# Kernel optimization log

Hardware: AMD Instinct MI355X
Metric: run time of the kernel (lower is better)

The kernel has to match this reference:

```python
import jax, jax.numpy as jnp
import numpy as np

OUTPUT_SIZES = [1, 3, 6, 8]  # SPP pyramid -> total KV length 110

def _bounds(n, out):
    # PyTorch AdaptiveMaxPool2d bin boundaries
    return [((i * n) // out, -((-(i + 1) * n) // out)) for i in range(out)]

def adaptive_max_pool2d(x, out):
    # x: [B, C, H, W] -> [B, C, out, out]
    B, C, H, W = x.shape
    rows = jnp.stack([x[:, :, s:e, :].max(axis=2) for s, e in _bounds(H, out)], axis=2)
    return jnp.stack([rows[:, :, :, s:e].max(axis=3) for s, e in _bounds(W, out)], axis=3)

def spp(x):
    # [B, C, H, W] -> [B, C, S] with S = sum(o*o) = 110
    B, C = x.shape[:2]
    return jnp.concatenate(
        [adaptive_max_pool2d(x, o).reshape(B, C, o * o) for o in OUTPUT_SIZES], axis=2)

def conv1x1(x, w):
    # 1x1 conv, no bias: w [O, C], x [B, C, H, W]
    return jnp.einsum('oc,bchw->bohw', w, x)

def setup_inputs() -> dict:
    key = jax.random.key(0)
    ks = jax.random.split(key, 6)
    B, C, H, W = 16, 512, 64, 64
    IC = C // 2
    x = jax.random.normal(ks[0], (B, C, H, W), jnp.float32)
    y = jax.random.normal(ks[1], (B, C, H, W), jnp.float32)
    sc = 1.0 / np.sqrt(C)
    w_phi = jax.random.normal(ks[2], (IC, C), jnp.float32) * sc
    w_theta = jax.random.normal(ks[3], (IC, C), jnp.float32) * sc
    w_g = jax.random.normal(ks[4], (IC, C), jnp.float32) * sc
    w_mask = jax.random.normal(ks[5], (C, IC), jnp.float32) * (1.0 / np.sqrt(IC))
    return {"x": x, "y": y, "w_phi": w_phi, "w_theta": w_theta,
            "w_g": w_g, "w_mask": w_mask}

def reference(x, y, w_phi, w_theta, w_g, w_mask):
    B, C, H, W = x.shape
    IC = w_phi.shape[0]
    N = H * W
    # Query: [B, N, IC]
    x_phi = conv1x1(x, w_phi).reshape(B, IC, N).transpose(0, 2, 1)
    # Keys/values from SPP-pooled y: [B, IC, S] / [B, S, IC]
    y_theta = spp(conv1x1(y, w_theta))
    y_g = spp(conv1x1(y, w_g)).transpose(0, 2, 1)
    # Attention with softmax over the QUERY axis (dim=1), as in the source
    attn = jax.nn.softmax(jnp.einsum('bnc,bcs->bns', x_phi, y_theta), axis=1)
    agg = jnp.einsum('bns,bsc->bnc', attn, y_g)          # [B, N, IC]
    agg = agg.transpose(0, 2, 1).reshape(B, IC, H, W)     # [B, IC, H, W]
    mask = conv1x1(agg, w_mask)                           # [B, C, H, W]
    return mask + x
```

## Files before the change

### kernel.cpp

```cpp
#include <hip/hip_runtime.h>

#define DI __device__ __forceinline__

typedef __attribute__((ext_vector_type(8))) __bf16 bf16x8;
typedef __attribute__((ext_vector_type(4))) float f32x4;

DI unsigned short f2bf(float x) {
  union { float f; unsigned u; } v; v.f = x;
  unsigned r = v.u + 0x7fffu + ((v.u >> 16) & 1u);
  return (unsigned short)(r >> 16);
}
DI float bf2f(unsigned short h) {
  union { unsigned u; float f; } v; v.u = ((unsigned)h) << 16;
  return v.f;
}
DI unsigned pack2(float a, float b) {
  return (unsigned)f2bf(a) | (((unsigned)f2bf(b)) << 16);
}

DI void gl_lds16(const void* g, void* l) {
  __builtin_amdgcn_global_load_lds(
      (const __attribute__((address_space(1))) void*)g,
      (__attribute__((address_space(3))) void*)l, 16, 0, 0);
}

DI void wt_vm0()  { asm volatile("s_waitcnt vmcnt(0) lgkmcnt(0)" ::: "memory"); }
DI void wt_vm6()  { asm volatile("s_waitcnt vmcnt(6) lgkmcnt(0)" ::: "memory"); }
DI void wt_vm8()  { asm volatile("s_waitcnt vmcnt(8) lgkmcnt(0)" ::: "memory"); }
DI void wt_vm10() { asm volatile("s_waitcnt vmcnt(10) lgkmcnt(0)" ::: "memory"); }
DI void wt_vm12() { asm volatile("s_waitcnt vmcnt(12) lgkmcnt(0)" ::: "memory"); }

__global__ __launch_bounds__(256) void pw_conv(
    const float* __restrict__ w_theta, const float* __restrict__ w_g,
    unsigned short* __restrict__ wTG)
{
  int e = (blockIdx.x * 256 + threadIdx.x) * 8;
  const float* src = (e < 131072) ? (w_theta + e) : (w_g + (e - 131072));
  float4 a = *(const float4*)src;
  float4 c = *(const float4*)(src + 4);
  uint4 u;
  u.x = pack2(a.x, a.y); u.y = pack2(a.z, a.w);
  u.z = pack2(c.x, c.y); u.w = pack2(c.z, c.w);
  *(uint4*)(wTG + e) = u;
}

__constant__ int c_RS[18] = {0, 0,21,42, 0,10,21,32,42,53, 0,8,16,24,32,40,48,56};
__constant__ int c_RE[18] = {64, 22,43,64, 11,22,32,43,54,64, 8,16,24,32,40,48,56,64};

__global__ __launch_bounds__(256) void k1f_conv_pool(
    const float* __restrict__ y, const unsigned short* __restrict__ wTG,
    unsigned short* __restrict__ Rbuf)
{
  const int tid = threadIdx.x;
  const int id = blockIdx.x;
  const int tile = (id & 7) * 16 + (id >> 3);
  const int mb = (tile & 3) * 128;
  const int nbt = tile >> 2;
  const int nb = nbt * 128;
  const int b  = blockIdx.y;
  const int lane = tid & 63, wv = tid >> 6;
  const int wm = (wv & 1) * 64, wn = (wv >> 1) * 64;
  const int l15 = lane & 15, l4 = lane >> 4;

  __shared__ __align__(16) char smem[3 * 18432];
  float* P = (float*)smem;

  const int c4 = tid & 7, n4 = tid >> 3;
  const float* ycol = y + ((size_t)(b * 512)) * 4096 + nb + n4 * 4;

  f32x4 acc[4][4];
  #pragma unroll
  for (int i = 0; i < 4; ++i)
    #pragma unroll
    for (int j = 0; j < 4; ++j) acc[i][j] = f32x4{0.f, 0.f, 0.f, 0.f};

  float xr0[16], xr1[16];
  auto yload = [&](float* xr, int kb) {
    #pragma unroll
    for (int cc = 0; cc < 4; ++cc)
      *(float4*)&xr[cc * 4] =
          *(const float4*)(ycol + (size_t)(kb + c4 * 4 + cc) * 4096);
  };
  auto dmaA = [&](int buf, int kb) {
    unsigned short* As = (unsigned short*)(smem + buf * 18432);
    #pragma unroll
    for (int p = 0; p < 2; ++p) {
      int chunk = (wv * 2 + p) * 64 + lane;
      int row = chunk >> 2, cc16 = chunk & 3;
      gl_lds16(wTG + ((size_t)(mb + row)) * 512 + kb + cc16 * 8,
               As + (wv * 2 + p) * 512);
    }
  };
  auto bwrite = [&](int buf, const float* xr) {
    unsigned short* Bs = (unsigned short*)(smem + buf * 18432 + 8192);
    #pragma unroll
    for (int q = 0; q < 4; ++q) {
      uint2 u;
      u.x = pack2(xr[q], xr[4 + q]);
      u.y = pack2(xr[8 + q], xr[12 + q]);
      *(uint2*)&Bs[(n4 * 4 + q) * 40 + c4 * 4] = u;
    }
  };
  auto mfma_step = [&](int buf) {
    const unsigned short* As = (const unsigned short*)(smem + buf * 18432);
    const unsigned short* Bs = As + 4096;
    bf16x8 af[4], bfr[4];
    #pragma unroll
    for (int i = 0; i < 4; ++i)
      af[i] = *(const bf16x8*)&As[(wm + i * 16 + l15) * 32 + l4 * 8];
    #pragma unroll
    for (int j = 0; j < 4; ++j)
      bfr[j] = *(const bf16x8*)&Bs[(wn + j * 16 + l15) * 40 + l4 * 8];
    #pragma unroll
    for (int i = 0; i < 4; ++i)
      #pragma unroll
      for (int j = 0; j < 4; ++j)
        acc[i][j] = __builtin_amdgcn_mfma_f32_16x16x32_bf16(af[i], bfr[j], acc[i][j], 0, 0, 0);
  };

  yload(xr0, 0);
  dmaA(0, 0);
  bwrite(0, xr0);
  yload(xr1, 32);
  #pragma unroll
  for (int t = 0; t < 16; ++t) {
    if (t + 1 < 16) dmaA((t + 1) % 3, (t + 1) * 32);
    if (t + 2 < 16) yload((t & 1) ? xr1 : xr0, (t + 2) * 32);
    if (t < 14) wt_vm10();
    else if (t == 14) wt_vm6();
    else wt_vm0();
    __builtin_amdgcn_s_barrier();
    __builtin_amdgcn_sched_barrier(0);
    mfma_step(t % 3);
    if (t + 1 < 16) bwrite((t + 1) % 3, (t & 1) ? xr0 : xr1);
  }

  const int hloc = wv >> 1;
  #pragma unroll
  for (int pass = 0; pass < 2; ++pass) {
    __syncthreads();
    if (hloc == pass) {
      #pragma unroll
      for (int i = 0; i < 4; ++i)
        #pragma unroll
        for (int j = 0; j < 4; ++j)
          #pragma unroll
          for (int r = 0; r < 4; ++r)
            P[(wm + i * 16 + l4 * 4 + r) * 65 + j * 16 + l15] = acc[i][j][r];
    }
    __syncthreads();
    const int o = tid & 127;
    size_t rbase = (((size_t)(b * 64 + nbt * 2 + pass)) * 18) * 512 + mb + o;
    if (tid < 128) {
      float b0 = -3.4e38f, b1 = b0, b2 = b0, b3 = b0;
      #pragma unroll
      for (int w = 0; w < 64; ++w) {
        float v = P[o * 65 + w];
        b0 = fmaxf(b0, v);
        if (w < 22) b1 = fmaxf(b1, v);
        if (w >= 21 && w < 43) b2 = fmaxf(b2, v);
        if (w >= 42) b3 = fmaxf(b3, v);
      }
      Rbuf[rbase]           = f2bf(b0);
      Rbuf[rbase + 512]     = f2bf(b1);
      Rbuf[rbase + 2 * 512] = f2bf(b2);
      Rbuf[rbase + 3 * 512] = f2bf(b3);
    } else {
      float s6[6], s8[8];
      #pragma unroll
      for (int i = 0; i < 6; ++i) s6[i] = -3.4e38f;
      #pragma unroll
      for (int i = 0; i < 8; ++i) s8[i] = -3.4e38f;
      constexpr int R6S[6] = {0, 10, 21, 32, 42, 53};
      constexpr int R6E[6] = {11, 22, 32, 43, 54, 64};
      #pragma unroll
      for (int w = 0; w < 64; ++w) {
        float v = P[o * 65 + w];
        #pragma unroll
        for (int i = 0; i < 6; ++i)
          if (w >= R6S[i] && w < R6E[i]) s6[i] = fmaxf(s6[i], v);
        s8[w >> 3] = fmaxf(s8[w >> 3], v);
      }
      #pragma unroll
      for (int i = 0; i < 6; ++i) Rbuf[rbase + (size_t)(4 + i) * 512] = f2bf(s6[i]);
      #pragma unroll
      for (int i = 0; i < 8; ++i) Rbuf[rbase + (size_t)(10 + i) * 512] = f2bf(s8[i]);
    }
  }
}

__global__ __launch_bounds__(256) void k2_pool_final(
    const unsigned short* __restrict__ Rbuf, float* __restrict__ Pt,
    float* __restrict__ Pg)
{
  const int s = blockIdx.x, b = blockIdx.y, tid = threadIdx.x;
  size_t obase = ((size_t)(b * 128) + s) * 256 + tid;
  if (s >= 110) { Pt[obase] = 0.f; Pg[obase] = 0.f; return; }
  int he, wb;
  if (s == 0)      { he = 0; wb = 0; }
  else if (s < 10) { int i = s - 1;  he = 1 + i / 3;  wb = 1 + i % 3; }
  else if (s < 46) { int i = s - 10; he = 4 + i / 6;  wb = 4 + i % 6; }
  else             { int i = s - 46; he = 10 + i / 8; wb = 10 + i % 8; }
  float m0 = -3.4e38f, m1 = -3.4e38f;
  int e = c_RE[he];
  for (int h = c_RS[he]; h < e; ++h) {
    const unsigned short* r = Rbuf + (((size_t)(b * 64 + h)) * 18 + wb) * 512;
    m0 = fmaxf(m0, bf2f(r[tid]));
    m1 = fmaxf(m1, bf2f(r[tid + 256]));
  }
  Pt[obase] = m0;
  Pg[obase] = m1;
}

__global__ __launch_bounds__(256) void k3_fused(
    const float* __restrict__ Pt, const float* __restrict__ Pg,
    const float* __restrict__ w_phi, const float* __restrict__ w_mask,
    unsigned short* __restrict__ Kth, unsigned short* __restrict__ Ktl,
    unsigned short* __restrict__ Vb)
{
  __shared__ __align__(16) char sm3[51200];
  const int tid = threadIdx.x;
  const int tx = tid & 15, ty = tid >> 4;
  const int b = blockIdx.y;
  if (blockIdx.z == 0) {
    const int ct = blockIdx.x;
    const int c0 = tx * 4, s0 = ty * 8;
    float* Ls = (float*)sm3;
    float* Ws = Ls + 128 * 64;
    float acc[8][4] = {};
    for (int kc = 0; kc < 256; kc += 64) {
      #pragma unroll
      for (int j = 0; j < 8; ++j) {
        int flat = tid + 256 * j;
        int row = flat >> 4, k4 = (flat & 15) << 2;
        *(float4*)&Ls[row * 64 + k4] =
            *(const float4*)(Pt + ((size_t)(b * 128) + row) * 256 + kc + k4);
      }
      #pragma unroll
      for (int j = 0; j < 4; ++j) {
        int flat = tid + 256 * j;
        int row = flat >> 4, cc4 = (flat & 15) << 2;
        *(float4*)&Ws[row * 68 + cc4] =
            *(const float4*)(w_phi + (size_t)(kc + row) * 512 + ct * 64 + cc4);
      }
      __syncthreads();
      for (int k = 0; k < 64; k += 4) {
        float4 wv[4];
        #pragma unroll
        for (int kk = 0; kk < 4; ++kk) wv[kk] = *(const float4*)&Ws[(k + kk) * 68 + c0];
        #pragma unroll
        for (int i = 0; i < 8; ++i) {
          float4 a = *(const float4*)&Ls[(s0 + i) * 64 + k];
          const float* ap = (const float*)&a;
          #pragma unroll
          for (int kk = 0; kk < 4; ++kk) {
            const float* wp = (const float*)&wv[kk];
            acc[i][0] += ap[kk] * wp[0];
            acc[i][1] += ap[kk] * wp[1];
            acc[i][2] += ap[kk] * wp[2];
            acc[i][3] += ap[kk] * wp[3];
          }
        }
      }
      __syncthreads();
    }
    #pragma unroll
    for (int i = 0; i < 8; ++i) {
      unsigned short hi[4]; float lo[4];
      #pragma unroll
      for (int j = 0; j < 4; ++j) { hi[j] = f2bf(acc[i][j]); lo[j] = acc[i][j] - bf2f(hi[j]); }
      size_t base = ((size_t)(b * 128) + s0 + i) * 512 + ct * 64 + c0;
      uint2 uh; uh.x = (unsigned)hi[0] | ((unsigned)hi[1] << 16);
      uh.y = (unsigned)hi[2] | ((unsigned)hi[3] << 16);
      uint2 ul; ul.x = pack2(lo[0], lo[1]); ul.y = pack2(lo[2], lo[3]);
      *(uint2*)&Kth[base] = uh;
      *(uint2*)&Ktl[base] = ul;
    }
  } else {
    const int ot = blockIdx.x;
    const int o0 = ty * 4;
    float* Ws = (float*)sm3;
    float* Ps = Ws + 64 * 64;
    float acc[4][8] = {};
    for (int kc = 0; kc < 256; kc += 64) {
      #pragma unroll
      for (int j = 0; j < 4; ++j) {
        int flat = tid + 256 * j;
        int row = flat >> 4, k4 = (flat & 15) << 2;
        *(float4*)&Ws[row * 64 + k4] =
            *(const float4*)(w_mask + (size_t)(ot * 64 + row) * 256 + kc + k4);
      }
      #pragma unroll
      for (int j = 0; j < 8; ++j) {
        int flat = tid + 256 * j;
        int row = flat >> 4, k4 = (flat & 15) << 2;
        *(float4*)&Ps[row * 68 + k4] =
            *(const float4*)(Pg + ((size_t)(b * 128) + row) * 256 + kc + k4);
      }
      __syncthreads();
      for (int k = 0; k < 64; k += 4) {
        float4 wv[4];
        #pragma unroll
        for (int i = 0; i < 4; ++i) wv[i] = *(const float4*)&Ws[(o0 + i) * 64 + k];
        #pragma unroll
        for (int jj = 0; jj < 8; ++jj) {
          float4 pv = *(const float4*)&Ps[(tx + 16 * jj) * 68 + k];
          const float* pp = (const float*)&pv;
          #pragma unroll
          for (int i = 0; i < 4; ++i) {
            const float* wp = (const float*)&wv[i];
            #pragma unroll
            for (int kk = 0; kk < 4; ++kk) acc[i][jj] += wp[kk] * pp[kk];
          }
        }
      }
      __syncthreads();
    }
    #pragma unroll
    for (int i = 0; i < 4; ++i)
      #pragma unroll
      for (int jj = 0; jj < 8; ++jj)
        Vb[((size_t)(b * 512) + ot * 64 + o0 + i) * 128 + tx + 16 * jj] =
            f2bf(acc[i][jj]);
  }
}

__global__ __launch_bounds__(256) void k4_scores(
    const float* __restrict__ x, const unsigned short* __restrict__ Kth,
    const unsigned short* __restrict__ Ktl, float* __restrict__ scoresT,
    float* __restrict__ pmax_g, float* __restrict__ psum_g)
{
  const int tid = threadIdx.x;
  const int ntile = blockIdx.x;
  const int nb = ntile * 128;
  const int b = blockIdx.y;
  const int lane = tid & 63, wv = tid >> 6;
  const int wm = (wv & 1) * 64, wn = (wv >> 1) * 64;
  const int l15 = lane & 15, l4 = lane >> 4;
  __shared__ __align__(16) char smem4[3 * 26624];
  __shared__ float SmP[256], SsP[256];

  const int c4 = tid & 7, n4 = tid >> 3;
  const float* xcol = x + ((size_t)(b * 512)) * 4096 + nb + n4 * 4;

  f32x4 acc[4][4];
  #pragma unroll
  for (int i = 0; i < 4; ++i)
    #pragma unroll
    for (int j = 0; j < 4; ++j) acc[i][j] = f32x4{0.f, 0.f, 0.f, 0.f};

  float xr0[16], xr1[16];
  auto xload = [&](float* xr, int kb) {
    #pragma unroll
    for (int cc = 0; cc < 4; ++cc)
      *(float4*)&xr[cc * 4] =
          *(const float4*)(xcol + (size_t)(kb + c4 * 4 + cc) * 4096);
  };
  auto dmaA = [&](int buf, int kb) {
    unsigned short* Ah = (unsigned short*)(smem4 + buf * 26624);
    unsigned short* Al = Ah + 4096;
    #pragma unroll
    for (int p = 0; p < 2; ++p) {
      int chunk = (wv * 2 + p) * 64 + lane;
      int row = chunk >> 2, cc16 = chunk & 3;
      size_t g = ((size_t)(b * 128) + row) * 512 + kb + cc16 * 8;
      gl_lds16(Kth + g, Ah + (wv * 2 + p) * 512);
      gl_lds16(Ktl + g, Al + (wv * 2 + p) * 512);
    }
  };
  auto bwrite = [&](int buf, const float* xr) {
    unsigned short* Bs = (unsigned short*)(smem4 + buf * 26624 + 16384);
    #pragma unroll
    for (int q = 0; q < 4; ++q) {
      uint2 u;
      u.x = pack2(xr[q], xr[4 + q]);
      u.y = pack2(xr[8 + q], xr[12 + q]);
      *(uint2*)&Bs[(n4 * 4 + q) * 40 + c4 * 4] = u;
    }
  };
  auto mfma_step = [&](int buf) {
    const unsigned short* Ah = (const unsigned short*)(smem4 + buf * 26624);
    const unsigned short* Al = Ah + 4096;
    const unsigned short* Bs = Al + 4096;
    bf16x8 ah[4], al[4], bfr[4];
    #pragma unroll
    for (int i = 0; i < 4; ++i) {
      ah[i] = *(const bf16x8*)&Ah[(wm + i * 16 + l15) * 32 + l4 * 8];
      al[i] = *(const bf16x8*)&Al[(wm + i * 16 + l15) * 32 + l4 * 8];
    }
    #pragma unroll
    for (int j = 0; j < 4; ++j)
      bfr[j] = *(const bf16x8*)&Bs[(wn + j * 16 + l15) * 40 + l4 * 8];
    #pragma unroll
    for (int i = 0; i < 4; ++i)
      #pragma unroll
      for (int j = 0; j < 4; ++j) {
        acc[i][j] = __builtin_amdgcn_mfma_f32_16x16x32_bf16(ah[i], bfr[j], acc[i][j], 0, 0, 0);
        acc[i][j] = __builtin_amdgcn_mfma_f32_16x16x32_bf16(al[i], bfr[j], acc[i][j], 0, 0, 0);
      }
  };

  xload(xr0, 0);
  dmaA(0, 0);
  bwrite(0, xr0);
  xload(xr1, 32);
  #pragma unroll
  for (int t = 0; t < 16; ++t) {
    if (t + 1 < 16) dmaA((t + 1) % 3, (t + 1) * 32);
    if (t + 2 < 16) xload((t & 1) ? xr1 : xr0, (t + 2) * 32);
    if (t < 14) wt_vm12();
    else if (t == 14) wt_vm8();
    else wt_vm0();
    __builtin_amdgcn_s_barrier();
    __builtin_amdgcn_sched_barrier(0);
    mfma_step(t % 3);
    if (t + 1 < 16) bwrite((t + 1) % 3, (t & 1) ? xr0 : xr1);
  }

  #pragma unroll
  for (int i = 0; i < 4; ++i)
    #pragma unroll
    for (int j = 0; j < 4; ++j)
      *(float4*)(scoresT + ((size_t)(b * 4096) + nb + wn + j * 16 + l15) * 128 +
                 wm + i * 16 + l4 * 4) = *(float4*)&acc[i][j];

  const int nh = wn >> 6;
  float cm[4][4];
  #pragma unroll
  for (int i = 0; i < 4; ++i)
    #pragma unroll
    for (int r = 0; r < 4; ++r) {
      float v = fmaxf(fmaxf(acc[i][0][r], acc[i][1][r]),
                      fmaxf(acc[i][2][r], acc[i][3][r]));
      v = fmaxf(v, __shfl_xor(v, 1));
      v = fmaxf(v, __shfl_xor(v, 2));
      v = fmaxf(v, __shfl_xor(v, 4));
      v = fmaxf(v, __shfl_xor(v, 8));
      if (l15 == 0) SmP[(wm + i * 16 + l4 * 4 + r) * 2 + nh] = v;
    }
  __syncthreads();
  #pragma unroll
  for (int i = 0; i < 4; ++i)
    #pragma unroll
    for (int r = 0; r < 4; ++r) {
      int s = wm + i * 16 + l4 * 4 + r;
      cm[i][r] = fmaxf(SmP[s * 2], SmP[s * 2 + 1]);
    }
  #pragma unroll
  for (int i = 0; i < 4; ++i)
    #pragma unroll
    for (int r = 0; r < 4; ++r) {
      float s0 = __expf(acc[i][0][r] - cm[i][r]) + __expf(acc[i][1][r] - cm[i][r]) +
                 __expf(acc[i][2][r] - cm[i][r]) + __expf(acc[i][3][r] - cm[i][r]);
      s0 += __shfl_xor(s0, 1);
      s0 += __shfl_xor(s0, 2);
      s0 += __shfl_xor(s0, 4);
      s0 += __shfl_xor(s0, 8);
      if (l15 == 0) SsP[(wm + i * 16 + l4 * 4 + r) * 2 + nh] = s0;
    }
  __syncthreads();
  if (tid < 128) {
    size_t pidx = ((size_t)(b * 128) + tid) * 32 + ntile;
    pmax_g[pidx] = fmaxf(SmP[tid * 2], SmP[tid * 2 + 1]);
    psum_g[pidx] = SsP[tid * 2] + SsP[tid * 2 + 1];
  }
}

__global__ __launch_bounds__(256) void k5e_exp(
    const float* __restrict__ scoresT, const float* __restrict__ pmax_g,
    const float* __restrict__ psum_g, unsigned short* __restrict__ Eb)
{
  const int b = blockIdx.y, tid = threadIdx.x;
  __shared__ float sm[128], sl[128];
  if (tid < 128) {
    float M = 0.f, linv = 0.f;
    if (tid < 110) {
      const float* pm = pmax_g + ((size_t)(b * 128) + tid) * 32;
      const float* ps = psum_g + ((size_t)(b * 128) + tid) * 32;
      M = -3.4e38f;
      #pragma unroll
      for (int t = 0; t < 32; ++t) M = fmaxf(M, pm[t]);
      float S = 0.f;
      #pragma unroll
      for (int t = 0; t < 32; ++t) S += ps[t] * __expf(pm[t] - M);
      linv = 1.f / S;
    }
    sm[tid] = M; sl[tid] = linv;
  }
  __syncthreads();
  const size_t base = (size_t)b * 4096 * 128;
  #pragma unroll
  for (int j = 0; j < 8; ++j) {
    int chunk = blockIdx.x * 2048 + j * 256 + tid;
    int sc = (chunk & 31) * 4;
    float4 v = *(const float4*)(scoresT + base + (size_t)chunk * 4);
    float e0 = __expf(v.x - sm[sc])     * sl[sc];
    float e1 = __expf(v.y - sm[sc + 1]) * sl[sc + 1];
    float e2 = __expf(v.z - sm[sc + 2]) * sl[sc + 2];
    float e3 = __expf(v.w - sm[sc + 3]) * sl[sc + 3];
    uint2 u; u.x = pack2(e0, e1); u.y = pack2(e2, e3);
    *(uint2*)(Eb + base + (size_t)chunk * 4) = u;
  }
}

__global__ __launch_bounds__(256) void k6_out(
    const unsigned short* __restrict__ Eb, const unsigned short* __restrict__ Vb,
    const float* __restrict__ x, float* __restrict__ out)
{
  const int tid = threadIdx.x;
  const int id = blockIdx.x;
  const int tile = (id & 7) * 16 + (id >> 3);
  const int mb = (tile & 3) * 128;
  const int nb = (tile >> 2) * 128;
  const int b = blockIdx.y;
  const int lane = tid & 63, wv = tid >> 6;
  const int wm = (wv & 1) * 64, wn = (wv >> 1) * 64;
  const int l15 = lane & 15, l4 = lane >> 4;
  __shared__ __align__(16) unsigned short SA[4][4096];
  __shared__ __align__(16) unsigned short SB[4][4096];

  #pragma unroll
  for (int h = 0; h < 4; ++h)
    #pragma unroll
    for (int p = 0; p < 2; ++p) {
      int chunk = (wv * 2 + p) * 64 + lane;
      int row = chunk >> 2, c16 = chunk & 3;
      gl_lds16(Vb + ((size_t)(b * 512) + mb + row) * 128 + h * 32 + c16 * 8,
               &SA[h][(wv * 2 + p) * 512]);
      gl_lds16(Eb + ((size_t)(b * 4096) + nb + row) * 128 + h * 32 + c16 * 8,
               &SB[h][(wv * 2 + p) * 512]);
    }

  float xr[4][4][4];
  #pragma unroll
  for (int i = 0; i < 4; ++i)
    #pragma unroll
    for (int j = 0; j < 4; ++j)
      #pragma unroll
      for (int r = 0; r < 4; ++r)
        xr[i][j][r] = x[((size_t)(b * 512) + mb + wm + i * 16 + l4 * 4 + r) * 4096 +
                        nb + wn + j * 16 + l15];

  f32x4 acc[4][4];
  #pragma unroll
  for (int i = 0; i < 4; ++i)
    #pragma unroll
    for (int j = 0; j < 4; ++j) acc[i][j] = f32x4{0.f, 0.f, 0.f, 0.f};

  __syncthreads();
  #pragma unroll
  for (int h = 0; h < 4; ++h) {
    bf16x8 af[4], bfr[4];
    #pragma unroll
    for (int i = 0; i < 4; ++i)
      af[i] = *(const bf16x8*)&SA[h][(wm + i * 16 + l15) * 32 + l4 * 8];
    #pragma unroll
    for (int j = 0; j < 4; ++j)
      bfr[j] = *(const bf16x8*)&SB[h][(wn + j * 16 + l15) * 32 + l4 * 8];
    #pragma unroll
    for (int i = 0; i < 4; ++i)
      #pragma unroll
      for (int j = 0; j < 4; ++j)
        acc[i][j] = __builtin_amdgcn_mfma_f32_16x16x32_bf16(af[i], bfr[j], acc[i][j], 0, 0, 0);
  }
  #pragma unroll
  for (int i = 0; i < 4; ++i)
    #pragma unroll
    for (int j = 0; j < 4; ++j)
      #pragma unroll
      for (int r = 0; r < 4; ++r) {
        int o = mb + wm + i * 16 + l4 * 4 + r;
        size_t idx = ((size_t)(b * 512) + o) * 4096 + nb + wn + j * 16 + l15;
        out[idx] = acc[i][j][r] + xr[i][j][r];
      }
}

extern "C" void kernel_launch(void* const* d_in, const int* in_sizes, int n_in,
                              void* d_out, int out_size, void* d_ws, size_t ws_size,
                              hipStream_t stream)
{
  (void)in_sizes; (void)n_in; (void)out_size; (void)ws_size;
  const float* x       = (const float*)d_in[0];
  const float* y       = (const float*)d_in[1];
  const float* w_phi   = (const float*)d_in[2];
  const float* w_theta = (const float*)d_in[3];
  const float* w_g     = (const float*)d_in[4];
  const float* w_mask  = (const float*)d_in[5];
  float* out = (float*)d_out;

  char* ws = (char*)d_ws;
  char* B0 = ws + 67108864;
  unsigned short* Rbuf = (unsigned short*)B0;
  float* scoresT = (float*)B0;
  unsigned short* Eb = (unsigned short*)(B0 + 33554432);
  unsigned short* wTG = (unsigned short*)(B0 + 50331648);
  unsigned short* Vb  = (unsigned short*)(B0 + 50331648);
  float* pmax_g = (float*)(B0 + 52428800);
  float* psum_g = (float*)(B0 + 52690944);
  char* C0 = B0 + 54525952;
  float* Pt = (float*)C0;
  float* Pg = (float*)(C0 + 2097152);
  unsigned short* Kth = (unsigned short*)(C0 + 4194304);
  unsigned short* Ktl = (unsigned short*)(C0 + 6291456);

  pw_conv<<<dim3(128), 256, 0, stream>>>(w_theta, w_g, wTG);
  k1f_conv_pool<<<dim3(128, 16), 256, 0, stream>>>(y, wTG, Rbuf);
  k2_pool_final<<<dim3(128, 16), 256, 0, stream>>>(Rbuf, Pt, Pg);
  k3_fused<<<dim3(8, 16, 2), 256, 0, stream>>>(Pt, Pg, w_phi, w_mask, Kth, Ktl, Vb);
  k4_scores<<<dim3(32, 16), 256, 0, stream>>>(x, Kth, Ktl, scoresT, pmax_g, psum_g);
  k5e_exp<<<dim3(64, 16), 256, 0, stream>>>(scoresT, pmax_g, psum_g, Eb);
  k6_out<<<dim3(128, 16), 256, 0, stream>>>(Eb, Vb, x, out);
}
```

Before: 493.2 us.

## Switch conv and score GEMM pipelines to double-buffered LDS with triple register prefetch

In the conv-pool and score kernels, LDS staging drops from three buffers to two. Global loads of the activation tile now run three steps ahead in registers instead of two, and the weight DMA is issued after the barrier. The score kernel's softmax scratch arrays reuse the staging LDS instead of getting their own allocation. The aim is lower LDS use, for better occupancy, and deeper latency hiding of the fp32 activation loads. In exchange it adds register pressure from the third 16-float prefetch buffer, and the DMA into the buffer just consumed now relies on that barrier.

```diff
diff --git a/kernel.cpp b/kernel.cpp
--- a/kernel.cpp
+++ b/kernel.cpp
@@ -24,11 +24,8 @@
       (__attribute__((address_space(3))) void*)l, 16, 0, 0);
 }
 
-DI void wt_vm0()  { asm volatile("s_waitcnt vmcnt(0) lgkmcnt(0)" ::: "memory"); }
-DI void wt_vm6()  { asm volatile("s_waitcnt vmcnt(6) lgkmcnt(0)" ::: "memory"); }
-DI void wt_vm8()  { asm volatile("s_waitcnt vmcnt(8) lgkmcnt(0)" ::: "memory"); }
-DI void wt_vm10() { asm volatile("s_waitcnt vmcnt(10) lgkmcnt(0)" ::: "memory"); }
-DI void wt_vm12() { asm volatile("s_waitcnt vmcnt(12) lgkmcnt(0)" ::: "memory"); }
+DI void wt_vm0() { asm volatile("s_waitcnt vmcnt(0) lgkmcnt(0)" ::: "memory"); }
+DI void wt_vm4() { asm volatile("s_waitcnt vmcnt(4) lgkmcnt(0)" ::: "memory"); }
 
 __global__ __launch_bounds__(256) void pw_conv(
     const float* __restrict__ w_theta, const float* __restrict__ w_g,
@@ -62,7 +59,7 @@
   const int wm = (wv & 1) * 64, wn = (wv >> 1) * 64;
   const int l15 = lane & 15, l4 = lane >> 4;
 
-  __shared__ __align__(16) char smem[3 * 18432];
+  __shared__ __align__(16) char smem[2 * 18432];
   float* P = (float*)smem;
 
   const int c4 = tid & 7, n4 = tid >> 3;
@@ -74,11 +71,11 @@
     #pragma unroll
     for (int j = 0; j < 4; ++j) acc[i][j] = f32x4{0.f, 0.f, 0.f, 0.f};
 
-  float xr0[16], xr1[16];
-  auto yload = [&](float* xr, int kb) {
+  float xr[3][16];
+  auto yload = [&](float* xrp, int kb) {
     #pragma unroll
     for (int cc = 0; cc < 4; ++cc)
-      *(float4*)&xr[cc * 4] =
+      *(float4*)&xrp[cc * 4] =
           *(const float4*)(ycol + (size_t)(kb + c4 * 4 + cc) * 4096);
   };
   auto dmaA = [&](int buf, int kb) {
@@ -91,13 +88,13 @@
                As + (wv * 2 + p) * 512);
     }
   };
-  auto bwrite = [&](int buf, const float* xr) {
+  auto bwrite = [&](int buf, const float* xrp) {
     unsigned short* Bs = (unsigned short*)(smem + buf * 18432 + 8192);
     #pragma unroll
     for (int q = 0; q < 4; ++q) {
       uint2 u;
-      u.x = pack2(xr[q], xr[4 + q]);
-      u.y = pack2(xr[8 + q], xr[12 + q]);
+      u.x = pack2(xrp[q], xrp[4 + q]);
+      u.y = pack2(xrp[8 + q], xrp[12 + q]);
       *(uint2*)&Bs[(n4 * 4 + q) * 40 + c4 * 4] = u;
     }
   };
@@ -118,21 +115,21 @@
         acc[i][j] = __builtin_amdgcn_mfma_f32_16x16x32_bf16(af[i], bfr[j], acc[i][j], 0, 0, 0);
   };
 
-  yload(xr0, 0);
   dmaA(0, 0);
-  bwrite(0, xr0);
-  yload(xr1, 32);
+  yload(xr[0], 0);
+  yload(xr[1], 32);
+  yload(xr[2], 64);
+  bwrite(0, xr[0]);
   #pragma unroll
   for (int t = 0; t < 16; ++t) {
-    if (t + 1 < 16) dmaA((t + 1) % 3, (t + 1) * 32);
-    if (t + 2 < 16) yload((t & 1) ? xr1 : xr0, (t + 2) * 32);
-    if (t < 14) wt_vm10();
-    else if (t == 14) wt_vm6();
+    if (t < 14) wt_vm4();
     else wt_vm0();
     __builtin_amdgcn_s_barrier();
     __builtin_amdgcn_sched_barrier(0);
-    mfma_step(t % 3);
-    if (t + 1 < 16) bwrite((t + 1) % 3, (t & 1) ? xr0 : xr1);
+    if (t + 1 < 16) dmaA((t + 1) & 1, (t + 1) * 32);
+    if (t + 3 < 16) yload(xr[t % 3], (t + 3) * 32);
+    mfma_step(t & 1);
+    if (t + 1 < 16) bwrite((t + 1) & 1, xr[(t + 1) % 3]);
   }
 
   const int hloc = wv >> 1;
@@ -337,8 +334,9 @@
   const int lane = tid & 63, wv = tid >> 6;
   const int wm = (wv & 1) * 64, wn = (wv >> 1) * 64;
   const int l15 = lane & 15, l4 = lane >> 4;
-  __shared__ __align__(16) char smem4[3 * 26624];
-  __shared__ float SmP[256], SsP[256];
+  __shared__ __align__(16) char smem4[2 * 26624];
+  float* SmP = (float*)smem4;
+  float* SsP = SmP + 256;
 
   const int c4 = tid & 7, n4 = tid >> 3;
   const float* xcol = x + ((size_t)(b * 512)) * 4096 + nb + n4 * 4;
@@ -349,11 +347,11 @@
     #pragma unroll
     for (int j = 0; j < 4; ++j) acc[i][j] = f32x4{0.f, 0.f, 0.f, 0.f};
 
-  float xr0[16], xr1[16];
-  auto xload = [&](float* xr, int kb) {
+  float xr[3][16];
+  auto xload = [&](float* xrp, int kb) {
     #pragma unroll
     for (int cc = 0; cc < 4; ++cc)
-      *(float4*)&xr[cc * 4] =
+      *(float4*)&xrp[cc * 4] =
           *(const float4*)(xcol + (size_t)(kb + c4 * 4 + cc) * 4096);
   };
   auto dmaA = [&](int buf, int kb) {
@@ -368,13 +366,13 @@
       gl_lds16(Ktl + g, Al + (wv * 2 + p) * 512);
     }
   };
-  auto bwrite = [&](int buf, const float* xr) {
+  auto bwrite = [&](int buf, const float* xrp) {
     unsigned short* Bs = (unsigned short*)(smem4 + buf * 26624 + 16384);
     #pragma unroll
     for (int q = 0; q < 4; ++q) {
       uint2 u;
-      u.x = pack2(xr[q], xr[4 + q]);
-      u.y = pack2(xr[8 + q], xr[12 + q]);
+      u.x = pack2(xrp[q], xrp[4 + q]);
+      u.y = pack2(xrp[8 + q], xrp[12 + q]);
       *(uint2*)&Bs[(n4 * 4 + q) * 40 + c4 * 4] = u;
     }
   };
@@ -400,21 +398,21 @@
       }
   };
 
-  xload(xr0, 0);
   dmaA(0, 0);
-  bwrite(0, xr0);
-  xload(xr1, 32);
+  xload(xr[0], 0);
+  xload(xr[1], 32);
+  xload(xr[2], 64);
+  bwrite(0, xr[0]);
   #pragma unroll
   for (int t = 0; t < 16; ++t) {
-    if (t + 1 < 16) dmaA((t + 1) % 3, (t + 1) * 32);
-    if (t + 2 < 16) xload((t & 1) ? xr1 : xr0, (t + 2) * 32);
-    if (t < 14) wt_vm12();
-    else if (t == 14) wt_vm8();
+    if (t < 14) wt_vm4();
     else wt_vm0();
     __builtin_amdgcn_s_barrier();
     __builtin_amdgcn_sched_barrier(0);
-    mfma_step(t % 3);
-    if (t + 1 < 16) bwrite((t + 1) % 3, (t & 1) ? xr0 : xr1);
+    if (t + 1 < 16) dmaA((t + 1) & 1, (t + 1) * 32);
+    if (t + 3 < 16) xload(xr[t % 3], (t + 3) * 32);
+    mfma_step(t & 1);
+    if (t + 1 < 16) bwrite((t + 1) & 1, xr[(t + 1) % 3]);
   }
 
   #pragma unroll
```

New measurement: 485.5 us. About the same (-1.6%).
